# Performance work log

Hardware: AMD Instinct MI355X
Metric: run time of the kernel (lower is better)

Reference implementation:

```python
import jax, jax.numpy as jnp
import numpy as np

B, S, H, E, D = 4, 4096, 1024, 8, 256

def setup_inputs() -> dict:
    key = jax.random.key(0)
    k0, k1, k2, k3, k4 = jax.random.split(key, 5)
    scale_h = 1.0 / np.sqrt(H)
    scale_d = 1.0 / np.sqrt(D)
    return {
        "x": jax.random.normal(k0, (B, S, H), dtype=jnp.float32),
        "gate_w": jax.random.normal(k1, (E, H), dtype=jnp.float32) * scale_h,  # nn.Linear(H,E) weight [E,H]
        "wg": jax.random.normal(k2, (E, H, D), dtype=jnp.float32) * scale_h,   # gate_proj per expert
        "wu": jax.random.normal(k3, (E, H, D), dtype=jnp.float32) * scale_h,   # up_proj per expert
        "wd": jax.random.normal(k4, (E, D, H), dtype=jnp.float32) * scale_d,   # down_proj per expert
    }

def reference(x, gate_w, wg, wu, wd):
    b, s, h = x.shape
    xf = x.reshape(-1, h)                                   # [T, H]
    logits = jnp.einsum('th,eh->te', xf, gate_w)            # router logits
    expert_idx = jnp.argmax(logits, axis=-1)                # top-1 expert per token
    onehot = jax.nn.one_hot(expert_idx, gate_w.shape[0], dtype=x.dtype)  # [T, E]
    g = jnp.einsum('th,ehd->etd', xf, wg)                   # [E, T, D]
    u = jnp.einsum('th,ehd->etd', xf, wu)                   # [E, T, D]
    inter = jnp.square(jax.nn.relu(g)) * u                  # ReLU^2 * up
    inter = inter * onehot.T[:, :, None]                    # zero out non-selected (expert, token) pairs
    out = jnp.einsum('etd,edh->th', inter, wd)              # combine over experts
    return out.reshape(b, s, h)
```

## Files before the change

kernel.cpp:

```cpp
#include <hip/hip_runtime.h>
#include <hip/hip_bf16.h>

#define TOK 16384
#define HD  1024
#define DD  256
#define NE  8

typedef __attribute__((ext_vector_type(8))) short short8;
typedef __attribute__((ext_vector_type(4))) float floatx4;
typedef unsigned short u16;

static __device__ __forceinline__ u16 f2bf(float f) {
  __hip_bfloat16 h = __float2bfloat16(f);
  return *reinterpret_cast<u16*>(&h);
}
static __device__ __forceinline__ short8 cvt8(const float* p) {
  float4 a = *(const float4*)p;
  float4 b = *(const float4*)(p + 4);
  u16 t[8] = {f2bf(a.x), f2bf(a.y), f2bf(a.z), f2bf(a.w),
              f2bf(b.x), f2bf(b.y), f2bf(b.z), f2bf(b.w)};
  return *(short8*)t;
}

static __device__ __forceinline__ void gl16(const u16* g, u16* l) {
  __builtin_amdgcn_global_load_lds(
      (const __attribute__((address_space(1))) void*)g,
      (__attribute__((address_space(3))) void*)l, 16, 0, 0);
}

__global__ __launch_bounds__(256) void prep_kernel(
    const float* __restrict__ wg, const float* __restrict__ wu,
    const float* __restrict__ wd, const float* __restrict__ x,
    const float* __restrict__ gw,
    u16* __restrict__ wgT, u16* __restrict__ wuT, u16* __restrict__ wdT,
    u16* __restrict__ xbf,
    int* __restrict__ counts, int* __restrict__ tlist)
{
  __shared__ u16 tile[64][72];
  __shared__ int sexp[8];
  __shared__ int sbase[NE];
  int bid = blockIdx.x;
  int tid = threadIdx.x;

  if (bid < 1536) {
    const float* src; u16* dst; int R, C;
    if (bid < 512)       { src = wg; dst = wgT; R = HD; C = DD; }
    else if (bid < 1024) { src = wu; dst = wuT; R = HD; C = DD; bid -= 512; }
    else                 { src = wd; dst = wdT; R = DD; C = HD; bid -= 1024; }
    int e = bid >> 6, t = bid & 63;
    int ntc = C >> 6;
    int tr = t / ntc, tc = t % ntc;
    int r = tid >> 2, c0 = (tid & 3) * 16;
    const float* s = src + (size_t)e * R * C + (size_t)(tr * 64 + r) * C + tc * 64 + c0;
    *(short8*)&tile[r][c0]     = cvt8(s);
    *(short8*)&tile[r][c0 + 8] = cvt8(s + 8);
    __syncthreads();
    int c = tid >> 2, r0 = (tid & 3) * 16;
    alignas(16) u16 buf[16];
    for (int j = 0; j < 16; ++j) buf[j] = tile[r0 + j][c];
    u16* d = dst + (size_t)e * R * C + (size_t)(tc * 64 + c) * R + tr * 64 + r0;
    *(float4*)(d)     = *(const float4*)&buf[0];
    *(float4*)(d + 8) = *(const float4*)&buf[8];
    return;
  }

  int lane = tid & 63, wave = tid >> 6;
  int tok0 = (bid - 1536) * 8;
  for (int i = 0; i < 2; ++i) {
    int li = wave * 2 + i;
    int t = tok0 + li;
    const float* xp = x + (size_t)t * HD + lane * 16;
    float4 x0 = *(const float4*)xp,       x1 = *(const float4*)(xp + 4);
    float4 x2 = *(const float4*)(xp + 8), x3 = *(const float4*)(xp + 12);
    {
      alignas(16) u16 b[16] = {
        f2bf(x0.x), f2bf(x0.y), f2bf(x0.z), f2bf(x0.w),
        f2bf(x1.x), f2bf(x1.y), f2bf(x1.z), f2bf(x1.w),
        f2bf(x2.x), f2bf(x2.y), f2bf(x2.z), f2bf(x2.w),
        f2bf(x3.x), f2bf(x3.y), f2bf(x3.z), f2bf(x3.w)};
      u16* xd = xbf + (size_t)t * HD + lane * 16;
      *(float4*)xd       = *(const float4*)&b[0];
      *(float4*)(xd + 8) = *(const float4*)&b[8];
    }
    float acc[NE];
    for (int e = 0; e < NE; ++e) {
      const float* gp = gw + e * HD + lane * 16;
      float4 g0 = *(const float4*)gp,       g1 = *(const float4*)(gp + 4);
      float4 g2 = *(const float4*)(gp + 8), g3 = *(const float4*)(gp + 12);
      acc[e] = x0.x*g0.x + x0.y*g0.y + x0.z*g0.z + x0.w*g0.w
             + x1.x*g1.x + x1.y*g1.y + x1.z*g1.z + x1.w*g1.w
             + x2.x*g2.x + x2.y*g2.y + x2.z*g2.z + x2.w*g2.w
             + x3.x*g3.x + x3.y*g3.y + x3.z*g3.z + x3.w*g3.w;
    }
    for (int off = 32; off >= 1; off >>= 1)
      for (int e = 0; e < NE; ++e) acc[e] += __shfl_xor(acc[e], off, 64);
    if (lane == 0) {
      int be = 0; float bv = acc[0];
      for (int e = 1; e < NE; ++e) if (acc[e] > bv) { bv = acc[e]; be = e; }
      sexp[li] = be;
    }
  }
  __syncthreads();
  if (tid < NE) {
    int c = 0;
    for (int i = 0; i < 8; ++i) c += (sexp[i] == tid) ? 1 : 0;
    sbase[tid] = c ? atomicAdd(&counts[tid], c) : 0;
  }
  __syncthreads();
  if (tid < 8) {
    int e = sexp[tid], rank = 0;
    for (int i = 0; i < tid; ++i) rank += (sexp[i] == e) ? 1 : 0;
    tlist[e * TOK + sbase[e] + rank] = tok0 + tid;
  }
}


__global__ __launch_bounds__(256) void gemm1_kernel(
    const u16* __restrict__ xbf, const u16* __restrict__ wgT,
    const u16* __restrict__ wuT,
    const int* __restrict__ counts, const int* __restrict__ tlist,
    u16* __restrict__ inter)
{
  int bid = blockIdx.x;
  int e = bid & 7, q = (bid >> 3) & 3, tile = bid >> 5;
  int cnt = counts[e];
  int row0 = tile * 64;
  if (row0 >= cnt) return;

  __shared__ int stok[64];
  __shared__ __align__(16) u16 xA[2][64 * 32];
  __shared__ __align__(16) u16 sB[2][128 * 32];

  int tid = threadIdx.x, lane = tid & 63, wave = tid >> 6;
  if (tid < 64) {
    int r = row0 + tid;
    stok[tid] = tlist[e * TOK + (r < cnt ? r : cnt - 1)];
  }
  __syncthreads();
  int rmax = cnt - row0; if (rmax > 64) rmax = 64;

  int col = lane & 15, quad = lane >> 4;
  int soff = ((lane & 3) ^ ((lane >> 3) & 3)) * 8;
  int rsub = lane >> 2;
  int xsl8 = (quad ^ ((col >> 1) & 3)) * 8;

  const u16* aS = xbf + (size_t)stok[wave * 16 + rsub] * HD + soff;
  const u16* bS[2];
#pragma unroll
  for (int jj = 0; jj < 2; ++jj) {
    int r = wave * 32 + jj * 16 + rsub;
    bS[jj] = (r < 64)
        ? (wgT + ((size_t)e * DD + q * 64 + r) * HD + soff)
        : (wuT + ((size_t)e * DD + q * 64 + (r - 64)) * HD + soff);
  }

  floatx4 acc[4][2];
  floatx4 zz = {0.f, 0.f, 0.f, 0.f};
#pragma unroll
  for (int m = 0; m < 4; ++m)
#pragma unroll
    for (int j = 0; j < 2; ++j) acc[m][j] = zz;

  gl16(aS, &xA[0][wave * 512]);
#pragma unroll
  for (int jj = 0; jj < 2; ++jj) gl16(bS[jj], &sB[0][(wave * 2 + jj) * 512]);
  __syncthreads();

  for (int t = 0; t < HD / 32; ++t) {
    int b = t & 1;
    if (t + 1 < HD / 32) {
      int k1 = (t + 1) * 32;
      gl16(aS + k1, &xA[b ^ 1][wave * 512]);
#pragma unroll
      for (int jj = 0; jj < 2; ++jj) gl16(bS[jj] + k1, &sB[b ^ 1][(wave * 2 + jj) * 512]);
    }
    short8 af[4], bfr[2];
#pragma unroll
    for (int m = 0; m < 4; ++m)
      af[m] = *(const short8*)&xA[b][(m * 16 + col) * 32 + xsl8];
    bfr[0] = *(const short8*)&sB[b][(wave * 16 + col) * 32 + xsl8];
    bfr[1] = *(const short8*)&sB[b][(64 + wave * 16 + col) * 32 + xsl8];
#pragma unroll
    for (int m = 0; m < 4; ++m)
#pragma unroll
      for (int j = 0; j < 2; ++j)
        acc[m][j] = __builtin_amdgcn_mfma_f32_16x16x32_bf16(af[m], bfr[j], acc[m][j], 0, 0, 0);
    __syncthreads();
  }

#pragma unroll
  for (int m = 0; m < 4; ++m)
#pragma unroll
    for (int r = 0; r < 4; ++r) {
      int row = m * 16 + quad * 4 + r;
      if (row < rmax) {
        float g = acc[m][0][r]; g = g > 0.f ? g : 0.f;
        float u = acc[m][1][r];
        inter[(size_t)stok[row] * DD + q * 64 + wave * 16 + col] = f2bf(g * g * u);
      }
    }
}

__global__ __launch_bounds__(256) void gemm2_kernel(
    const u16* __restrict__ inter, const u16* __restrict__ wdT,
    const int* __restrict__ counts, const int* __restrict__ tlist,
    float* __restrict__ out)
{
  int bid = blockIdx.x;
  int e = bid & 7, q = (bid >> 3) & 7, tile = bid >> 6;
  int cnt = counts[e];
  int row0 = tile * 64;
  if (row0 >= cnt) return;
  int n0 = q * 128;

  __shared__ int stok[64];
  __shared__ __align__(16) u16 xA[2][64 * 32];
  __shared__ __align__(16) u16 sB[2][128 * 32];
  float (*st)[132] = (float(*)[132])&sB[0][0];

  int tid = threadIdx.x, lane = tid & 63, wave = tid >> 6;
  if (tid < 64) {
    int r = row0 + tid;
    stok[tid] = tlist[e * TOK + (r < cnt ? r : cnt - 1)];
  }
  __syncthreads();
  int rmax = cnt - row0; if (rmax > 64) rmax = 64;

  int col = lane & 15, quad = lane >> 4;
  int soff = ((lane & 3) ^ ((lane >> 3) & 3)) * 8;
  int rsub = lane >> 2;
  int xsl8 = (quad ^ ((col >> 1) & 3)) * 8;

  const u16* aS = inter + (size_t)stok[wave * 16 + rsub] * DD + soff;
  const u16* bS[2];
#pragma unroll
  for (int jj = 0; jj < 2; ++jj) {
    int r = wave * 32 + jj * 16 + rsub;
    bS[jj] = wdT + ((size_t)e * HD + n0 + r) * DD + soff;
  }

  floatx4 acc[4][2];
  floatx4 zz = {0.f, 0.f, 0.f, 0.f};
#pragma unroll
  for (int m = 0; m < 4; ++m)
#pragma unroll
    for (int j = 0; j < 2; ++j) acc[m][j] = zz;

  gl16(aS, &xA[0][wave * 512]);
#pragma unroll
  for (int jj = 0; jj < 2; ++jj) gl16(bS[jj], &sB[0][(wave * 2 + jj) * 512]);
  __syncthreads();

  for (int t = 0; t < DD / 32; ++t) {
    int b = t & 1;
    if (t + 1 < DD / 32) {
      int k1 = (t + 1) * 32;
      gl16(aS + k1, &xA[b ^ 1][wave * 512]);
#pragma unroll
      for (int jj = 0; jj < 2; ++jj) gl16(bS[jj] + k1, &sB[b ^ 1][(wave * 2 + jj) * 512]);
    }
    short8 af[4], bfr[2];
#pragma unroll
    for (int m = 0; m < 4; ++m)
      af[m] = *(const short8*)&xA[b][(m * 16 + col) * 32 + xsl8];
#pragma unroll
    for (int j = 0; j < 2; ++j)
      bfr[j] = *(const short8*)&sB[b][(wave * 32 + j * 16 + col) * 32 + xsl8];
#pragma unroll
    for (int m = 0; m < 4; ++m)
#pragma unroll
      for (int j = 0; j < 2; ++j)
        acc[m][j] = __builtin_amdgcn_mfma_f32_16x16x32_bf16(af[m], bfr[j], acc[m][j], 0, 0, 0);
    __syncthreads();
  }

  for (int m = 0; m < 4; ++m) {
    __syncthreads();
#pragma unroll
    for (int j = 0; j < 2; ++j)
#pragma unroll
      for (int r = 0; r < 4; ++r)
        st[quad * 4 + r][wave * 32 + j * 16 + col] = acc[m][j][r];
    __syncthreads();
#pragma unroll
    for (int i = 0; i < 2; ++i) {
      int id = i * 256 + tid;
      int r = id >> 5, c4 = (id & 31) * 4;
      int row = m * 16 + r;
      if (row < rmax)
        *(float4*)(out + (size_t)stok[row] * HD + n0 + c4) = *(const float4*)&st[r][c4];
    }
  }
}

extern "C" void kernel_launch(void* const* d_in, const int* in_sizes, int n_in,
                              void* d_out, int out_size, void* d_ws, size_t ws_size,
                              hipStream_t stream) {
  const float* x  = (const float*)d_in[0];
  const float* gw = (const float*)d_in[1];
  const float* wg = (const float*)d_in[2];
  const float* wu = (const float*)d_in[3];
  const float* wd = (const float*)d_in[4];
  float* out = (float*)d_out;

  char* ws = (char*)d_ws;
  int* counts = (int*)ws;
  int* tlist  = (int*)(ws + 256);
  u16* wgT   = (u16*)(ws + 524544);
  u16* wuT   = wgT + (size_t)NE * DD * HD;
  u16* wdT   = wuT + (size_t)NE * DD * HD;
  u16* inter = wdT + (size_t)NE * HD * DD;
  u16* xbf   = (u16*)d_out;

  hipMemsetAsync(counts, 0, NE * sizeof(int), stream);
  prep_kernel<<<1536 + TOK / 8, 256, 0, stream>>>(wg, wu, wd, x, gw,
                                                  wgT, wuT, wdT, xbf, counts, tlist);
  gemm1_kernel<<<8192, 256, 0, stream>>>(xbf, wgT, wuT, counts, tlist, inter);
  gemm2_kernel<<<16384, 256, 0, stream>>>(inter, wdT, counts, tlist, out);
}
```

Before: 231.4 us.

## Replace atomic token bucketing with per-block histograms and a prefix-scan scatter kernel

```diff
diff --git a/kernel.cpp b/kernel.cpp
--- a/kernel.cpp
+++ b/kernel.cpp
@@ -34,11 +34,10 @@
     const float* __restrict__ gw,
     u16* __restrict__ wgT, u16* __restrict__ wuT, u16* __restrict__ wdT,
     u16* __restrict__ xbf,
-    int* __restrict__ counts, int* __restrict__ tlist)
+    int* __restrict__ hcnt, int* __restrict__ eid)
 {
   __shared__ u16 tile[64][72];
-  __shared__ int sexp[8];
-  __shared__ int sbase[NE];
+  __shared__ int sexp[16];
   int bid = blockIdx.x;
   int tid = threadIdx.x;
 
@@ -65,52 +64,102 @@
   }
 
   int lane = tid & 63, wave = tid >> 6;
-  int tok0 = (bid - 1536) * 8;
-  for (int i = 0; i < 2; ++i) {
-    int li = wave * 2 + i;
-    int t = tok0 + li;
-    const float* xp = x + (size_t)t * HD + lane * 16;
-    float4 x0 = *(const float4*)xp,       x1 = *(const float4*)(xp + 4);
-    float4 x2 = *(const float4*)(xp + 8), x3 = *(const float4*)(xp + 12);
-    {
-      alignas(16) u16 b[16] = {
-        f2bf(x0.x), f2bf(x0.y), f2bf(x0.z), f2bf(x0.w),
-        f2bf(x1.x), f2bf(x1.y), f2bf(x1.z), f2bf(x1.w),
-        f2bf(x2.x), f2bf(x2.y), f2bf(x2.z), f2bf(x2.w),
-        f2bf(x3.x), f2bf(x3.y), f2bf(x3.z), f2bf(x3.w)};
-      u16* xd = xbf + (size_t)t * HD + lane * 16;
-      *(float4*)xd       = *(const float4*)&b[0];
-      *(float4*)(xd + 8) = *(const float4*)&b[8];
-    }
-    float acc[NE];
-    for (int e = 0; e < NE; ++e) {
-      const float* gp = gw + e * HD + lane * 16;
-      float4 g0 = *(const float4*)gp,       g1 = *(const float4*)(gp + 4);
-      float4 g2 = *(const float4*)(gp + 8), g3 = *(const float4*)(gp + 12);
-      acc[e] = x0.x*g0.x + x0.y*g0.y + x0.z*g0.z + x0.w*g0.w
-             + x1.x*g1.x + x1.y*g1.y + x1.z*g1.z + x1.w*g1.w
-             + x2.x*g2.x + x2.y*g2.y + x2.z*g2.z + x2.w*g2.w
-             + x3.x*g3.x + x3.y*g3.y + x3.z*g3.z + x3.w*g3.w;
-    }
-    for (int off = 32; off >= 1; off >>= 1)
-      for (int e = 0; e < NE; ++e) acc[e] += __shfl_xor(acc[e], off, 64);
-    if (lane == 0) {
-      int be = 0; float bv = acc[0];
-      for (int e = 1; e < NE; ++e) if (acc[e] > bv) { bv = acc[e]; be = e; }
-      sexp[li] = be;
+  int rb = bid - 1536;
+  int tok0 = rb * 16 + wave * 4;
+  float4 xr[4][4];
+#pragma unroll
+  for (int t = 0; t < 4; ++t) {
+    const float* xp = x + (size_t)(tok0 + t) * HD + lane * 16;
+    xr[t][0] = *(const float4*)xp;
+    xr[t][1] = *(const float4*)(xp + 4);
+    xr[t][2] = *(const float4*)(xp + 8);
+    xr[t][3] = *(const float4*)(xp + 12);
+  }
+#pragma unroll
+  for (int t = 0; t < 4; ++t) {
+    alignas(16) u16 b[16] = {
+      f2bf(xr[t][0].x), f2bf(xr[t][0].y), f2bf(xr[t][0].z), f2bf(xr[t][0].w),
+      f2bf(xr[t][1].x), f2bf(xr[t][1].y), f2bf(xr[t][1].z), f2bf(xr[t][1].w),
+      f2bf(xr[t][2].x), f2bf(xr[t][2].y), f2bf(xr[t][2].z), f2bf(xr[t][2].w),
+      f2bf(xr[t][3].x), f2bf(xr[t][3].y), f2bf(xr[t][3].z), f2bf(xr[t][3].w)};
+    u16* xd = xbf + (size_t)(tok0 + t) * HD + lane * 16;
+    *(float4*)xd       = *(const float4*)&b[0];
+    *(float4*)(xd + 8) = *(const float4*)&b[8];
+  }
+  float acc[4][NE];
+#pragma unroll
+  for (int e = 0; e < NE; ++e) {
+    const float* gp = gw + e * HD + lane * 16;
+    float4 g0 = *(const float4*)gp,       g1 = *(const float4*)(gp + 4);
+    float4 g2 = *(const float4*)(gp + 8), g3 = *(const float4*)(gp + 12);
+#pragma unroll
+    for (int t = 0; t < 4; ++t) {
+      acc[t][e] = xr[t][0].x*g0.x + xr[t][0].y*g0.y + xr[t][0].z*g0.z + xr[t][0].w*g0.w
+                + xr[t][1].x*g1.x + xr[t][1].y*g1.y + xr[t][1].z*g1.z + xr[t][1].w*g1.w
+                + xr[t][2].x*g2.x + xr[t][2].y*g2.y + xr[t][2].z*g2.z + xr[t][2].w*g2.w
+                + xr[t][3].x*g3.x + xr[t][3].y*g3.y + xr[t][3].z*g3.z + xr[t][3].w*g3.w;
+    }
+  }
+  for (int off = 32; off >= 1; off >>= 1)
+#pragma unroll
+    for (int t = 0; t < 4; ++t)
+#pragma unroll
+      for (int e = 0; e < NE; ++e) acc[t][e] += __shfl_xor(acc[t][e], off, 64);
+  if (lane == 0) {
+#pragma unroll
+    for (int t = 0; t < 4; ++t) {
+      int be = 0; float bv = acc[t][0];
+      for (int e = 1; e < NE; ++e) if (acc[t][e] > bv) { bv = acc[t][e]; be = e; }
+      sexp[wave * 4 + t] = be;
     }
   }
   __syncthreads();
   if (tid < NE) {
     int c = 0;
-    for (int i = 0; i < 8; ++i) c += (sexp[i] == tid) ? 1 : 0;
-    sbase[tid] = c ? atomicAdd(&counts[tid], c) : 0;
-  }
-  __syncthreads();
-  if (tid < 8) {
-    int e = sexp[tid], rank = 0;
-    for (int i = 0; i < tid; ++i) rank += (sexp[i] == e) ? 1 : 0;
-    tlist[e * TOK + sbase[e] + rank] = tok0 + tid;
+    for (int i = 0; i < 16; ++i) c += (sexp[i] == tid) ? 1 : 0;
+    hcnt[tid * 1024 + rb] = c;
+  }
+  if (tid < 16) eid[rb * 16 + tid] = sexp[tid];
+}
+
+__global__ __launch_bounds__(256) void scatter_kernel(
+    const int* __restrict__ eid, const int* __restrict__ hcnt,
+    int* __restrict__ counts, int* __restrict__ tlist)
+{
+  __shared__ int seid[64];
+  __shared__ int sp[NE][33];
+  __shared__ int sbase0[NE];
+  int bid = blockIdx.x, tid = threadIdx.x;
+  int t0 = bid * 64;
+  if (tid < 64) seid[tid] = eid[t0 + tid];
+  int e = tid >> 5, i = tid & 31;
+  int lim = 4 * bid;
+  int s = 0;
+  for (int c = i; c < lim; c += 32) s += hcnt[e * 1024 + c];
+  sp[e][i] = s;
+  __syncthreads();
+  if (tid < NE) {
+    int b = 0;
+    for (int j = 0; j < 32; ++j) b += sp[tid][j];
+    sbase0[tid] = b;
+  }
+  if (bid == 0) {
+    int st = 0;
+    for (int c = i; c < 1024; c += 32) st += hcnt[e * 1024 + c];
+    __syncthreads();
+    sp[e][i] = st;
+    __syncthreads();
+    if (tid < NE) {
+      int b = 0;
+      for (int j = 0; j < 32; ++j) b += sp[tid][j];
+      counts[tid] = b;
+    }
+  }
+  __syncthreads();
+  if (tid < 64) {
+    int ee = seid[tid], rank = 0;
+    for (int j = 0; j < tid; ++j) rank += (seid[j] == ee) ? 1 : 0;
+    tlist[ee * TOK + sbase0[ee] + rank] = t0 + tid;
   }
 }
 
@@ -310,11 +359,13 @@
   u16* wuT   = wgT + (size_t)NE * DD * HD;
   u16* wdT   = wuT + (size_t)NE * DD * HD;
   u16* inter = wdT + (size_t)NE * HD * DD;
+  int* eid   = (int*)(inter + (size_t)TOK * DD);
+  int* hcnt  = eid + TOK;
   u16* xbf   = (u16*)d_out;
 
-  hipMemsetAsync(counts, 0, NE * sizeof(int), stream);
-  prep_kernel<<<1536 + TOK / 8, 256, 0, stream>>>(wg, wu, wd, x, gw,
-                                                  wgT, wuT, wdT, xbf, counts, tlist);
+  prep_kernel<<<2560, 256, 0, stream>>>(wg, wu, wd, x, gw,
+                                        wgT, wuT, wdT, xbf, hcnt, eid);
+  scatter_kernel<<<256, 256, 0, stream>>>(eid, hcnt, counts, tlist);
   gemm1_kernel<<<8192, 256, 0, stream>>>(xbf, wgT, wuT, counts, tlist, inter);
   gemm2_kernel<<<16384, 256, 0, stream>>>(inter, wdT, counts, tlist, out);
 }
```

New measurement: 216.8 us. 6.3% less time.
